# Optimization experiments

Hardware: AMD Instinct MI355X
Metric: run time of the kernel (lower is better)

The kernel has to match this reference:

```python
import jax, jax.numpy as jnp
import numpy as np

IN_FEATURES = 4096
OUT_FEATURES = 11008
GROUP_SIZE = 128
NUM_GROUPS = IN_FEATURES // GROUP_SIZE  # 32


def setup_inputs() -> dict:
    key = jax.random.key(0)
    k1, k2, k3, k4 = jax.random.split(key, 4)
    x = jax.random.normal(k1, (8192, IN_FEATURES), dtype=jnp.float32)
    # packed 4-bit weights: one uint8 byte holds two 4-bit values
    qweight = jax.random.randint(k2, (IN_FEATURES * OUT_FEATURES // 2,), 0, 256, dtype=jnp.int32)
    qzeros = jax.random.randint(k3, (OUT_FEATURES, NUM_GROUPS), 0, 16, dtype=jnp.int32)
    scales = jax.random.uniform(k4, (OUT_FEATURES, NUM_GROUPS), dtype=jnp.float32) * 0.01
    return {"x": x, "qweight": qweight, "qzeros": qzeros, "scales": scales}


def _dequantize(qweight, qzeros, scales):
    # unpack: low nibble first, then high nibble (matches stack([low, high], dim=1).view(-1))
    b = qweight.astype(jnp.int32)
    low = b & 15
    high = (b >> 4) & 15
    w = jnp.stack([low, high], axis=1).reshape(-1)  # [in*out]
    w = w[: OUT_FEATURES * IN_FEATURES].reshape(OUT_FEATURES, IN_FEATURES).astype(jnp.float32)
    # per-group dequant: (w - zero) * scale, groups along in_features
    w = w.reshape(OUT_FEATURES, NUM_GROUPS, GROUP_SIZE)
    w = (w - qzeros[:, :, None].astype(jnp.float32)) * scales[:, :, None]
    return w.reshape(OUT_FEATURES, IN_FEATURES)


def reference(x, qweight, qzeros, scales) -> jnp.ndarray:
    weight = _dequantize(qweight, qzeros, scales).astype(x.dtype)  # [out, in]
    # F.linear(x, W) = x @ W.T
    return jnp.einsum("bi,oi->bo", x, weight)
```

## Files before the change

### kernel.cpp

```cpp
#include <hip/hip_runtime.h>
#include <hip/hip_bf16.h>


#define IN_F   4096
#define OUT_F  11008
#define M_DIM  8192
#define NGROUP 32

typedef __bf16 bf16x8 __attribute__((ext_vector_type(8)));
typedef float  f32x4  __attribute__((ext_vector_type(4)));
typedef unsigned short u16;
typedef u16 u16x8v __attribute__((ext_vector_type(8)));

__device__ __forceinline__ u16 f2bf(float f) {
  union { float f; unsigned u; } v; v.f = f;
  unsigned u = v.u;
  return (u16)((u + 0x7fffu + ((u >> 16) & 1u)) >> 16);
}

__device__ __forceinline__ void gload_lds16(const void* gsrc, void* ldst) {
  __builtin_amdgcn_global_load_lds(
      (const __attribute__((address_space(1))) void*)gsrc,
      (__attribute__((address_space(3))) void*)ldst, 16, 0, 0);
}

__global__ __launch_bounds__(256) void dequant_w(const int* __restrict__ qw,
                                                 const int* __restrict__ qz,
                                                 const float* __restrict__ sc,
                                                 u16* __restrict__ W) {
  const int total = (IN_F / 2) * OUT_F / 4;
  int stride = gridDim.x * blockDim.x;
  for (int idx = blockIdx.x * blockDim.x + threadIdx.x; idx < total; idx += stride) {
    int j = idx << 2;
    int o = j >> 11;
    int g = (j >> 6) & 31;
    float z = (float)qz[(o << 5) + g];
    float s = sc[(o << 5) + g];
    int4 q = ((const int4*)qw)[idx];
    int qs0 = q.x, qs1 = q.y, qs2 = q.z, qs3 = q.w;
    u16x8v w;
    w[0] = f2bf(((float)(qs0 & 15) - z) * s);
    w[1] = f2bf(((float)((qs0 >> 4) & 15) - z) * s);
    w[2] = f2bf(((float)(qs1 & 15) - z) * s);
    w[3] = f2bf(((float)((qs1 >> 4) & 15) - z) * s);
    w[4] = f2bf(((float)(qs2 & 15) - z) * s);
    w[5] = f2bf(((float)((qs2 >> 4) & 15) - z) * s);
    w[6] = f2bf(((float)(qs3 & 15) - z) * s);
    w[7] = f2bf(((float)((qs3 >> 4) & 15) - z) * s);
    ((u16x8v*)W)[idx] = w;
  }
}

__global__ __launch_bounds__(256) void cvt_x(const float* __restrict__ x,
                                             u16* __restrict__ Xb) {
  const int total = M_DIM * IN_F / 8;
  int stride = gridDim.x * blockDim.x;
  for (int idx = blockIdx.x * blockDim.x + threadIdx.x; idx < total; idx += stride) {
    float4 a = ((const float4*)x)[idx * 2];
    float4 b = ((const float4*)x)[idx * 2 + 1];
    u16x8v v;
    v[0] = f2bf(a.x); v[1] = f2bf(a.y); v[2] = f2bf(a.z); v[3] = f2bf(a.w);
    v[4] = f2bf(b.x); v[5] = f2bf(b.y); v[6] = f2bf(b.z); v[7] = f2bf(b.w);
    ((u16x8v*)Xb)[idx] = v;
  }
}


#define BAR       __builtin_amdgcn_s_barrier()
#define LGKM0     asm volatile("s_waitcnt lgkmcnt(0)" ::: "memory")
#define LGKM8     asm volatile("s_waitcnt lgkmcnt(8)" ::: "memory")
#define VMCNT6    asm volatile("s_waitcnt vmcnt(6)" ::: "memory")
#define PRIO(p)   __builtin_amdgcn_s_setprio(p)

__global__ __launch_bounds__(512, 2) void gemm256(const u16* __restrict__ A,
                                                  const u16* __restrict__ B,
                                                  float* __restrict__ C) {
  constexpr int K = IN_F, N = OUT_F;
  constexpr int NT = K / 64;
  __shared__ __align__(16) u16 sA[2][256 * 64];
  __shared__ __align__(16) u16 sB[2][256 * 64];

  const int NTN = OUT_F / 256;
  const int NWG = (M_DIM / 256) * NTN;
  int bid = blockIdx.x;
  int wg  = (bid & 7) * (NWG / 8) + (bid >> 3);
  int tm = wg / NTN, tn = wg - tm * NTN;
  int m0 = tm * 256, n0 = tn * 256;

  int tid  = threadIdx.x;
  int lane = tid & 63;
  int wave = tid >> 6;
  int wr = wave >> 2, wc = wave & 3;

  int rstage = tid >> 3;
  int gslot  = ((tid & 7) ^ (rstage & 7)) << 3;
  int ldsoff = rstage * 64 + ((tid & 7) << 3);
  const u16* Ag = A + (size_t)(m0 + rstage) * K + gslot;
  const u16* Bg = B + (size_t)(n0 + rstage) * K + gslot;

#define STAGE_A(cb, h, kt) do {                                   \
    const u16* _g = Ag + (size_t)(h) * 128 * K + (kt) * 64;       \
    u16* _l = sA[cb] + (h) * 128 * 64 + ldsoff;                   \
    gload_lds16(_g, _l);                                          \
    gload_lds16(_g + (size_t)64 * K, _l + 64 * 64);               \
  } while (0)

#define STAGE_B(cb, h, kt) do {                                   \
    const u16* _g = Bg + (size_t)(h) * 128 * K + (kt) * 64;       \
    u16* _l = sB[cb] + (h) * 128 * 64 + ldsoff;                   \
    gload_lds16(_g, _l);                                          \
    gload_lds16(_g + (size_t)64 * K, _l + 64 * 64);               \
  } while (0)

  int q8  = lane >> 4;
  int sl0 = ((q8 ^ (lane & 7)) << 3);
  int sl1 = (((q8 | 4) ^ (lane & 7)) << 3);
  int abase = (wr * 64 + (lane & 15)) * 64;
  int bbase = (wc * 32 + (lane & 15)) * 64;

  bf16x8 a_[8], b0_[4], b1_[4];
  f32x4 acc[8][4] = {};

#define LDA(cb, mh) do {                                          \
    const u16* _p = sA[cb] + abase + (mh) * 8192;                 \
    a_[0] = *(const bf16x8*)(_p + sl0);                           \
    a_[1] = *(const bf16x8*)(_p + sl1);                           \
    a_[2] = *(const bf16x8*)(_p + 1024 + sl0);                    \
    a_[3] = *(const bf16x8*)(_p + 1024 + sl1);                    \
    a_[4] = *(const bf16x8*)(_p + 2048 + sl0);                    \
    a_[5] = *(const bf16x8*)(_p + 2048 + sl1);                    \
    a_[6] = *(const bf16x8*)(_p + 3072 + sl0);                    \
    a_[7] = *(const bf16x8*)(_p + 3072 + sl1);                    \
  } while (0)

#define LDB(cb, nh, dst) do {                                     \
    const u16* _p = sB[cb] + bbase + (nh) * 8192;                 \
    dst[0] = *(const bf16x8*)(_p + sl0);                          \
    dst[1] = *(const bf16x8*)(_p + sl1);                          \
    dst[2] = *(const bf16x8*)(_p + 1024 + sl0);                   \
    dst[3] = *(const bf16x8*)(_p + 1024 + sl1);                   \
  } while (0)

#define QUAD(mh, nh, bq) do {                                                  \
    _Pragma("unroll") for (int mf = 0; mf < 4; mf++)                           \
      _Pragma("unroll") for (int nf = 0; nf < 2; nf++) {                       \
        acc[(mh)*4+mf][(nh)*2+nf] = __builtin_amdgcn_mfma_f32_16x16x32_bf16(   \
            a_[mf*2+0], bq[nf*2+0], acc[(mh)*4+mf][(nh)*2+nf], 0, 0, 0);       \
        acc[(mh)*4+mf][(nh)*2+nf] = __builtin_amdgcn_mfma_f32_16x16x32_bf16(   \
            a_[mf*2+1], bq[nf*2+1], acc[(mh)*4+mf][(nh)*2+nf], 0, 0, 0);       \
      }                                                                        \
  } while (0)

#define TILE(c, u) do {                                           \
    int _k1 = ((u) + 1) & (NT - 1), _k2 = ((u) + 2) & (NT - 1);   \
                         \
    LDA(c, 0); LDB(c, 0, b0_); STAGE_A((c) ^ 1, 1, _k1);          \
    LGKM8; BAR; LGKM0; PRIO(1); QUAD(0, 0, b0_); PRIO(0); BAR;    \
                           \
    LDB(c, 1, b1_); STAGE_A(c, 0, _k2);                           \
    BAR; LGKM0; PRIO(1); QUAD(0, 1, b1_); PRIO(0); BAR;           \
                           \
    LDA(c, 1); STAGE_B(c, 0, _k2);                                \
    BAR; LGKM0; PRIO(1); QUAD(1, 1, b1_); PRIO(0); BAR;           \
      \
    STAGE_B(c, 1, _k2);                                           \
    BAR; PRIO(1); QUAD(1, 0, b0_); PRIO(0); VMCNT6; BAR;          \
  } while (0)

  STAGE_A(0, 0, 0); STAGE_A(0, 1, 0);
  STAGE_B(0, 0, 0); STAGE_B(0, 1, 0);
  STAGE_A(1, 0, 1); STAGE_B(1, 0, 1); STAGE_B(1, 1, 1);
  VMCNT6; BAR;

#pragma unroll 1
  for (int u = 0; u < NT; u += 2) {
    TILE(0, u);
    TILE(1, u + 1);
  }

  float* Cp = C + (size_t)(m0 + wr * 64 + ((lane >> 4) << 2)) * N
                + n0 + wc * 32 + (lane & 15);
#pragma unroll
  for (int m = 0; m < 8; m++) {
    int roff = (m >> 2) * 128 + (m & 3) * 16;
#pragma unroll
    for (int n = 0; n < 4; n++) {
      int coff = (n >> 1) * 128 + (n & 1) * 16;
#pragma unroll
      for (int j = 0; j < 4; j++)
        Cp[(size_t)(roff + j) * N + coff] = acc[m][n][j];
    }
  }
}

__global__ __launch_bounds__(256) void naive_gemm(const float* __restrict__ x,
                                                  const int* __restrict__ qw,
                                                  const int* __restrict__ qz,
                                                  const float* __restrict__ sc,
                                                  float* __restrict__ out) {
  __shared__ float xs[IN_F];
  int m = blockIdx.y;
  int n = blockIdx.x * 256 + threadIdx.x;
  for (int i = threadIdx.x; i < IN_F; i += 256) xs[i] = x[(size_t)m * IN_F + i];
  __syncthreads();
  float acc = 0.f;
  const int* qrow = qw + (size_t)n * (IN_F / 2);
  for (int g = 0; g < NGROUP; g++) {
    float z = (float)qz[n * NGROUP + g];
    float s = sc[n * NGROUP + g];
    for (int t = 0; t < 64; t++) {
      int q = qrow[g * 64 + t];
      acc += xs[g * 128 + 2 * t] * ((float)(q & 15) - z) * s;
      acc += xs[g * 128 + 2 * t + 1] * ((float)((q >> 4) & 15) - z) * s;
    }
  }
  out[(size_t)m * OUT_F + n] = acc;
}

extern "C" void kernel_launch(void* const* d_in, const int* in_sizes, int n_in,
                              void* d_out, int out_size, void* d_ws, size_t ws_size,
                              hipStream_t stream) {
  const float* x  = (const float*)d_in[0];
  const int*   qw = (const int*)d_in[1];
  const int*   qz = (const int*)d_in[2];
  const float* sc = (const float*)d_in[3];
  float* out = (float*)d_out;

  const size_t WBYTES = (size_t)OUT_F * IN_F * 2;
  const size_t XBYTES = (size_t)M_DIM * IN_F * 2;

  if (ws_size >= WBYTES + XBYTES) {
    u16* Wb = (u16*)d_ws;
    u16* Xb = (u16*)((char*)d_ws + WBYTES);
    dequant_w<<<2048, 256, 0, stream>>>(qw, qz, sc, Wb);
    cvt_x<<<2048, 256, 0, stream>>>(x, Xb);
    gemm256<<<(M_DIM / 256) * (OUT_F / 256), 512, 0, stream>>>(Xb, Wb, out);
  } else {
    naive_gemm<<<dim3(OUT_F / 256, M_DIM), 256, 0, stream>>>(x, qw, qz, sc, out);
  }
}
```

Before: 788.6 us.

## Software-pipeline LDS fragment reads into MFMA quads across tile iterations

Restructures the per-tile schedule so LDS reads of the next A and B fragments are issued interleaved with the MFMA quads that consume the current fragments. The first fragments of the next tile are prefetched during the last quad, with a prologue load before the loop. The vmcnt wait moves to the third phase with a lower count. This aims to hide LDS latency behind MFMA work and drop the LGKM8 stall, but it raises register pressure and makes correctness depend on barrier ordering against staged buffers.

```diff
diff --git a/kernel.cpp b/kernel.cpp
--- a/kernel.cpp
+++ b/kernel.cpp
@@ -67,8 +67,9 @@
 
 
 #define BAR       __builtin_amdgcn_s_barrier()
+#define SCHED0    __builtin_amdgcn_sched_barrier(0)
 #define LGKM0     asm volatile("s_waitcnt lgkmcnt(0)" ::: "memory")
-#define LGKM8     asm volatile("s_waitcnt lgkmcnt(8)" ::: "memory")
+#define VMCNT4    asm volatile("s_waitcnt vmcnt(4)" ::: "memory")
 #define VMCNT6    asm volatile("s_waitcnt vmcnt(6)" ::: "memory")
 #define PRIO(p)   __builtin_amdgcn_s_setprio(p)
 
@@ -151,26 +152,53 @@
       }                                                                        \
   } while (0)
 
+#define QUAD_ROLLA(mh, nh, bq, rp) do {                                        \
+    _Pragma("unroll") for (int mf = 0; mf < 4; mf++) {                         \
+      _Pragma("unroll") for (int nf = 0; nf < 2; nf++) {                       \
+        acc[(mh)*4+mf][(nh)*2+nf] = __builtin_amdgcn_mfma_f32_16x16x32_bf16(   \
+            a_[mf*2+0], bq[nf*2+0], acc[(mh)*4+mf][(nh)*2+nf], 0, 0, 0);       \
+        acc[(mh)*4+mf][(nh)*2+nf] = __builtin_amdgcn_mfma_f32_16x16x32_bf16(   \
+            a_[mf*2+1], bq[nf*2+1], acc[(mh)*4+mf][(nh)*2+nf], 0, 0, 0);       \
+      }                                                                        \
+      a_[mf*2+0] = *(const bf16x8*)((rp) + mf * 1024 + sl0);                   \
+      a_[mf*2+1] = *(const bf16x8*)((rp) + mf * 1024 + sl1);                   \
+    }                                                                          \
+  } while (0)
+
 #define TILE(c, u) do {                                           \
     int _k1 = ((u) + 1) & (NT - 1), _k2 = ((u) + 2) & (NT - 1);   \
-                         \
-    LDA(c, 0); LDB(c, 0, b0_); STAGE_A((c) ^ 1, 1, _k1);          \
-    LGKM8; BAR; LGKM0; PRIO(1); QUAD(0, 0, b0_); PRIO(0); BAR;    \
-                           \
-    LDB(c, 1, b1_); STAGE_A(c, 0, _k2);                           \
-    BAR; LGKM0; PRIO(1); QUAD(0, 1, b1_); PRIO(0); BAR;           \
-                           \
-    LDA(c, 1); STAGE_B(c, 0, _k2);                                \
-    BAR; LGKM0; PRIO(1); QUAD(1, 1, b1_); PRIO(0); BAR;           \
-      \
+                                                          \
+    STAGE_A((c) ^ 1, 1, _k1);                                     \
+    BAR; LGKM0; PRIO(1);                                          \
+    LDB(c, 1, b1_);                                               \
+    QUAD(0, 0, b0_);                                              \
+    PRIO(0); BAR;                                                 \
+                                                          \
+    STAGE_A(c, 0, _k2);                                           \
+    BAR; LGKM0; PRIO(1);                                          \
+    QUAD_ROLLA(0, 1, b1_, sA[c] + abase + 8192);                  \
+    PRIO(0); BAR;                                                 \
+                                                          \
+    STAGE_B(c, 0, _k2);                                           \
+    BAR; LGKM0; PRIO(1);                                          \
+    QUAD(1, 0, b0_);                                              \
+    PRIO(0); VMCNT4; BAR;                                         \
+                                                          \
     STAGE_B(c, 1, _k2);                                           \
-    BAR; PRIO(1); QUAD(1, 0, b0_); PRIO(0); VMCNT6; BAR;          \
+    BAR; LGKM0; PRIO(1);                                          \
+    LDB((c) ^ 1, 0, b0_);                                         \
+    QUAD_ROLLA(1, 1, b1_, sA[(c) ^ 1] + abase);                   \
+    PRIO(0); BAR;                                                 \
   } while (0)
 
   STAGE_A(0, 0, 0); STAGE_A(0, 1, 0);
   STAGE_B(0, 0, 0); STAGE_B(0, 1, 0);
   STAGE_A(1, 0, 1); STAGE_B(1, 0, 1); STAGE_B(1, 1, 1);
   VMCNT6; BAR;
+  SCHED0;
+  asm volatile("" ::: "memory");
+  LDA(0, 0);
+  LDB(0, 0, b0_);
 
 #pragma unroll 1
   for (int u = 0; u < NT; u += 2) {
```

New measurement: 723.4 us. 8.3% less time.
